# Performance work log

Measured on AMD Instinct MI355X. Metric: run time of the kernel, lower is better.

## Reference

```python
import jax, jax.numpy as jnp
import numpy as np
import math

BS, S, D = 2, 2048, 2048
DOWN, UP, H, RD = 512, 1024, 16, 32
HD = D // H            # 128, used only in softmax scale
VD = UP // H           # 64 per-head value dim
CD = UP // H           # 64 per-head content q/k dim
SCALE = math.sqrt(HD) + math.sqrt(RD)


def _rope(x, head_dim):
    # x: [bs, heads, seq, head_dim]; standard rotate-half RoPE
    seq = x.shape[2]
    inv_freq = 1.0 / (10000.0 ** (jnp.arange(0, head_dim, 2, dtype=jnp.float32) / head_dim))
    freqs = jnp.arange(seq, dtype=jnp.float32)[:, None] * inv_freq[None, :]  # [S, hd/2]
    emb = jnp.concatenate([freqs, freqs], axis=-1)                            # [S, hd]
    cos = jnp.cos(emb)[None, None]
    sin = jnp.sin(emb)[None, None]
    x1, x2 = x[..., : head_dim // 2], x[..., head_dim // 2 :]
    rot = jnp.concatenate([-x2, x1], axis=-1)
    return x * cos + rot * sin


def setup_inputs() -> dict:
    key = jax.random.key(0)
    ks = jax.random.split(key, 10)
    sd = 0.02
    inp = {
        'h': jax.random.normal(ks[0], (BS, S, D), jnp.float32),
        'mask': jnp.tril(jnp.ones((1, 1, S, S), jnp.int32)),
        'Wdkv': jax.random.normal(ks[1], (DOWN, D), jnp.float32) * sd,
        'bdkv': jnp.zeros((DOWN,), jnp.float32),
        'Wuk': jax.random.normal(ks[2], (UP, DOWN), jnp.float32) * sd,
        'buk': jnp.zeros((UP,), jnp.float32),
        'Wuv': jax.random.normal(ks[3], (UP, DOWN), jnp.float32) * sd,
        'buv': jnp.zeros((UP,), jnp.float32),
        'Wdq': jax.random.normal(ks[4], (DOWN, D), jnp.float32) * sd,
        'bdq': jnp.zeros((DOWN,), jnp.float32),
        'Wuq': jax.random.normal(ks[5], (UP, DOWN), jnp.float32) * sd,
        'buq': jnp.zeros((UP,), jnp.float32),
        'Wqr': jax.random.normal(ks[6], (RD * H, DOWN), jnp.float32) * sd,
        'bqr': jnp.zeros((RD * H,), jnp.float32),
        'Wkr': jax.random.normal(ks[7], (RD, D), jnp.float32) * sd,
        'bkr': jnp.zeros((RD,), jnp.float32),
        'Wfc': jax.random.normal(ks[8], (D, H * VD), jnp.float32) * sd,
        'bfc': jnp.zeros((D,), jnp.float32),
    }
    return inp


def reference(h, mask, Wdkv, bdkv, Wuk, buk, Wuv, buv, Wdq, bdq, Wuq, buq,
              Wqr, bqr, Wkr, bkr, Wfc, bfc):
    bs, seq, _ = h.shape
    # low-rank KV path
    c_kv = h @ Wdkv.T + bdkv                                   # [bs,S,DOWN]
    k_c = (c_kv @ Wuk.T + buk).reshape(bs, seq, H, CD).transpose(0, 2, 1, 3)
    v_c = (c_kv @ Wuv.T + buv).reshape(bs, seq, H, VD).transpose(0, 2, 1, 3)
    # low-rank Q path
    c_q = h @ Wdq.T + bdq                                      # [bs,S,DOWN]
    q_c = (c_q @ Wuq.T + buq).reshape(bs, seq, H, CD).transpose(0, 2, 1, 3)
    # decoupled RoPE paths
    q_r = _rope((c_q @ Wqr.T + bqr).reshape(bs, seq, H, RD).transpose(0, 2, 1, 3), RD)
    k_r = _rope((h @ Wkr.T + bkr).reshape(bs, seq, 1, RD).transpose(0, 2, 1, 3), RD)
    k_r = jnp.broadcast_to(k_r, (bs, H, seq, RD))              # shared RoPE key across heads
    q = jnp.concatenate([q_c, q_r], axis=-1)                   # [bs,H,S,CD+RD]
    k = jnp.concatenate([k_c, k_r], axis=-1)
    scores = jnp.einsum('bhqd,bhkd->bhqk', q, k)
    # NB: original applies mask BEFORE dividing by scale
    scores = jnp.where(mask == 0, -1e9, scores)
    probs = jax.nn.softmax(scores / SCALE, axis=-1)
    out = jnp.einsum('bhqk,bhkd->bhqd', probs, v_c)            # [bs,H,S,VD]
    out = out.transpose(0, 2, 1, 3).reshape(bs, seq, H * VD)
    return out @ Wfc.T + bfc
```

## Files before the change

### kernel.cpp

```cpp
#include <hip/hip_runtime.h>
#include <hip/hip_bf16.h>
#include <math.h>

typedef unsigned short u16;
typedef __attribute__((ext_vector_type(8))) short bf16x8;
typedef __attribute__((ext_vector_type(4))) float f32x4;
typedef __attribute__((ext_vector_type(16))) float f32x16;

namespace {

constexpr int BS = 2;
constexpr int S = 2048;
constexpr int D = 2048;
constexpr int DOWN = 512;
constexpr int UP = 1024;
constexpr int H = 16;
constexpr int RD = 32;
constexpr int VD = 64;
constexpr int QKD = 96;
constexpr int M = BS * S;
constexpr int N1 = 1152;
constexpr int N2 = 2048;
constexpr int N3 = 1536;

__device__ __forceinline__ float b2f(u16 u) {
  unsigned int x = ((unsigned int)u) << 16;
  return __uint_as_float(x);
}
__device__ __forceinline__ u16 f2b(float f) {
  unsigned int u = __float_as_uint(f);
  u += 0x7fff + ((u >> 16) & 1);
  return (u16)(u >> 16);
}
__device__ __forceinline__ void store_out(float* p, float v) { *p = v; }
__device__ __forceinline__ void store_out(u16* p, float v) { *p = f2b(v); }

__device__ __forceinline__ void async16(const u16* g, u16* lds) {
  __builtin_amdgcn_global_load_lds(
      (const __attribute__((address_space(1))) unsigned int*)g,
      (__attribute__((address_space(3))) unsigned int*)lds, 16, 0, 0);
}

__device__ __forceinline__ float exp2_fast(float x) {
#if __has_builtin(__builtin_amdgcn_exp2f)
  return __builtin_amdgcn_exp2f(x);
#else
  float r;
  asm("v_exp_f32 %0, %1" : "=v"(r) : "v"(x));
  return r;
#endif
}

__device__ __forceinline__ unsigned pkbf(float a, float b) {
  union { __hip_bfloat162 h; unsigned u; } c;
  c.h = __float22bfloat162_rn(make_float2(a, b));
  return c.u;
}
__device__ __forceinline__ void plswap(unsigned& a, unsigned& b) {
  asm("v_permlane32_swap_b32 %0, %1" : "+v"(a), "+v"(b));
}

__device__ __forceinline__ f32x4 mfma32(bf16x8 a, bf16x8 b, f32x4 c) {
  return __builtin_amdgcn_mfma_f32_16x16x32_bf16(a, b, c, 0, 0, 0);
}
__device__ __forceinline__ f32x16 mfma3216(bf16x8 a, bf16x8 b, f32x16 c) {
  return __builtin_amdgcn_mfma_f32_32x32x16_bf16(a, b, c, 0, 0, 0);
}

__global__ __launch_bounds__(256) void prep_kernel(
    const float* __restrict__ h, const float* __restrict__ Wdkv,
    const float* __restrict__ Wdq, const float* __restrict__ Wkr,
    const float* __restrict__ Wuk, const float* __restrict__ Wuv,
    const float* __restrict__ Wuq, const float* __restrict__ Wqr,
    const float* __restrict__ Wfc, const float* __restrict__ bdkv,
    const float* __restrict__ bdq, const float* __restrict__ bkr,
    const float* __restrict__ buk, const float* __restrict__ buv,
    const float* __restrict__ buq, const float* __restrict__ bqr,
    u16* __restrict__ hb, u16* __restrict__ Wcat1, u16* __restrict__ Wcat2,
    u16* __restrict__ Wcat3, u16* __restrict__ Wfcb,
    float* __restrict__ bcat1, float* __restrict__ bcat2,
    float* __restrict__ bcat3, float* __restrict__ ct, float* __restrict__ st) {
  const long i = (long)blockIdx.x * 256 + threadIdx.x;
  if (i >= 3630240) return;
  if (i < 3620864) {
    const float* src; u16* dst; long off;
    if      (i < 2097152) { src = h;    dst = hb;              off = i; }
    else if (i < 2359296) { src = Wdkv; dst = Wcat1;           off = i - 2097152; }
    else if (i < 2621440) { src = Wdq;  dst = Wcat1 + 1048576; off = i - 2359296; }
    else if (i < 2637824) { src = Wkr;  dst = Wcat1 + 2097152; off = i - 2621440; }
    else if (i < 2768896) { src = Wuk;  dst = Wcat2;           off = i - 2637824; }
    else if (i < 2899968) { src = Wuv;  dst = Wcat2 + 524288;  off = i - 2768896; }
    else if (i < 3031040) { src = Wuq;  dst = Wcat3;           off = i - 2899968; }
    else if (i < 3096576) { src = Wqr;  dst = Wcat3 + 524288;  off = i - 3031040; }
    else                  { src = Wfc;  dst = Wfcb;            off = i - 3096576; }
    float4 v = ((const float4*)src)[off];
    ushort4 o;
    o.x = f2b(v.x); o.y = f2b(v.y); o.z = f2b(v.z); o.w = f2b(v.w);
    ((ushort4*)dst)[off] = o;
  } else if (i < 3622048) {
    long j0 = (i - 3620864) * 4;
#pragma unroll
    for (int e = 0; e < 4; ++e) {
      long j = j0 + e;
      if (j < N1) {
        float v = 0.f;
        if (j < 512) v = bdkv[j];
        else if (j < 1024) v = bdq[j - 512];
        else if (j < 1056) v = bkr[j - 1024];
        bcat1[j] = v;
      } else if (j < N1 + N2) {
        long jj = j - N1;
        bcat2[jj] = (jj < 1024) ? buk[jj] : buv[jj - 1024];
      } else {
        long jj = j - N1 - N2;
        bcat3[jj] = (jj < 1024) ? buq[jj] : bqr[jj - 1024];
      }
    }
  } else {
    long k0 = (i - 3622048) * 4;
#pragma unroll
    for (int e = 0; e < 4; ++e) {
      long k = k0 + e;
      int s = (int)(k >> 4), r = (int)(k & 15);
      float f = powf(10000.f, -(float)r / 16.f);
      float th = (float)s * f;
      ct[k] = cosf(th);
      st[k] = sinf(th);
    }
  }
}

template <int BN, typename OutT>
__device__ __forceinline__ void gemm_body(
    const u16* __restrict__ A, int lda, const u16* __restrict__ W, int ldw,
    const float* __restrict__ bias, OutT* __restrict__ C, int ldc, int K,
    int m0, int n0) {
  constexpr int NFR = BN / 32;
  __shared__ u16 As[128 * 32];
  __shared__ u16 Bs[BN * 32];
  const int t = threadIdx.x;
  const int lane = t & 63, wave = t >> 6;
  const int wm = (wave >> 1) * 64, wn = (wave & 1) * (BN / 2);
  const int lrow = lane & 15, lk = (lane >> 4) * 8;
  const int srow = lane >> 2, scol = (lane & 3) * 8;
  f32x4 acc[4][NFR] = {};
  for (int k0 = 0; k0 < K; k0 += 32) {
    __syncthreads();
    {
      int r = wave * 32 + srow;
      async16(A + (size_t)(m0 + r) * lda + k0 + scol, As + (wave * 32) * 32);
      async16(A + (size_t)(m0 + r + 16) * lda + k0 + scol,
              As + (wave * 32 + 16) * 32);
    }
    if (BN == 128) {
      int r = wave * 32 + srow;
      async16(W + (size_t)(n0 + r) * ldw + k0 + scol, Bs + (wave * 32) * 32);
      async16(W + (size_t)(n0 + r + 16) * ldw + k0 + scol,
              Bs + (wave * 32 + 16) * 32);
    } else {
      int r = wave * 16 + srow;
      async16(W + (size_t)(n0 + r) * ldw + k0 + scol, Bs + (wave * 16) * 32);
    }
    __syncthreads();
    bf16x8 af[4], bfr[NFR];
#pragma unroll
    for (int i = 0; i < 4; ++i)
      af[i] = *(const bf16x8*)(As + (wm + i * 16 + lrow) * 32 + lk);
#pragma unroll
    for (int i = 0; i < NFR; ++i)
      bfr[i] = *(const bf16x8*)(Bs + (wn + i * 16 + lrow) * 32 + lk);
#pragma unroll
    for (int mi = 0; mi < 4; ++mi)
#pragma unroll
      for (int ni = 0; ni < NFR; ++ni)
        acc[mi][ni] = mfma32(af[mi], bfr[ni], acc[mi][ni]);
  }
#pragma unroll
  for (int mi = 0; mi < 4; ++mi)
#pragma unroll
    for (int ni = 0; ni < NFR; ++ni)
#pragma unroll
      for (int r = 0; r < 4; ++r) {
        int m = m0 + wm + mi * 16 + (lane >> 4) * 4 + r;
        int n = n0 + wn + ni * 16 + lrow;
        store_out(C + (size_t)m * ldc + n, acc[mi][ni][r] + bias[n]);
      }
}

template <int BN, typename OutT>
__global__ __launch_bounds__(256) void gemm_bt_mfma(
    const u16* __restrict__ A, int lda, const u16* __restrict__ W, int ldw,
    const float* __restrict__ bias, OutT* __restrict__ C, int ldc, int K) {
  gemm_body<BN, OutT>(A, lda, W, ldw, bias, C, ldc, K,
                      blockIdx.x * 128, blockIdx.y * BN);
}

__global__ __launch_bounds__(256) void gemm_up_fused(
    const u16* __restrict__ C1v, const u16* __restrict__ Wcat2,
    const u16* __restrict__ Wcat3, const float* __restrict__ bcat2,
    const float* __restrict__ bcat3, u16* __restrict__ C2,
    u16* __restrict__ C3) {
  const int by = blockIdx.y;
  const u16* A;
  const u16* W;
  const float* bias;
  u16* C;
  int ldc, n0;
  if (by < 16) {
    A = C1v; W = Wcat2; bias = bcat2; C = C2; ldc = N2; n0 = by * 128;
  } else {
    A = C1v + DOWN; W = Wcat3; bias = bcat3; C = C3; ldc = N3;
    n0 = (by - 16) * 128;
  }
  gemm_body<128, u16>(A, N1, W, DOWN, bias, C, ldc, DOWN,
                      blockIdx.x * 128, n0);
}

__global__ __launch_bounds__(256) void transpose_kernel(
    const u16* __restrict__ in, int ld_in, u16* __restrict__ outT, int ld_out) {
  __shared__ u16 tile[64][72];
  const int m0 = blockIdx.x * 64, n0 = blockIdx.y * 64;
  const int r = threadIdx.x >> 2, c0 = (threadIdx.x & 3) * 16;
  *(bf16x8*)(&tile[r][c0]) =
      *(const bf16x8*)(in + (size_t)(m0 + r) * ld_in + n0 + c0);
  *(bf16x8*)(&tile[r][c0 + 8]) =
      *(const bf16x8*)(in + (size_t)(m0 + r) * ld_in + n0 + c0 + 8);
  __syncthreads();
  bf16x8 o0, o1;
#pragma unroll
  for (int j = 0; j < 8; ++j) {
    o0[j] = (short)tile[c0 + j][r];
    o1[j] = (short)tile[c0 + 8 + j][r];
  }
  *(bf16x8*)(outT + (size_t)(n0 + r) * ld_out + m0 + c0) = o0;
  *(bf16x8*)(outT + (size_t)(n0 + r) * ld_out + m0 + c0 + 8) = o1;
}

__global__ __launch_bounds__(192) void pack_q_kernel(
    const u16* __restrict__ qc, const u16* __restrict__ qr,
    const float* __restrict__ ct, const float* __restrict__ st,
    u16* __restrict__ Qp) {
  const int t = threadIdx.x;
  const int sub = (t >= 96) ? 1 : 0;
  const int d = t - sub * 96;
  const int s = blockIdx.x * 2 + sub, h = blockIdx.y, b = blockIdx.z;
  const float sc = 1.44269504088896f / (sqrtf(128.f) + sqrtf(32.f));
  float val;
  if (d < 64) {
    val = b2f(qc[(size_t)(b * S + s) * N3 + h * VD + d]);
  } else {
    int r = d - 64;
    const u16* qrow = qr + (size_t)(b * S + s) * N3 + h * RD;
    float x = b2f(qrow[r]), xp = b2f(qrow[r ^ 16]);
    float c = ct[s * 16 + (r & 15)], sn = st[s * 16 + (r & 15)];
    val = (r < 16) ? (x * c - xp * sn) : (x * c + xp * sn);
  }
  Qp[((size_t)(b * H + h) * S + s) * QKD + d] = f2b(val * sc);
}

__global__ __launch_bounds__(192) void pack_k_kernel(
    const u16* __restrict__ kc,
    const u16* __restrict__ kr,
    const float* __restrict__ ct, const float* __restrict__ st,
    u16* __restrict__ Kp) {
  const int t = threadIdx.x;
  const int sub = (t >= 96) ? 1 : 0;
  const int d = t - sub * 96;
  const int s = blockIdx.x * 2 + sub, h = blockIdx.y, b = blockIdx.z;
  float val;
  if (d < 64) {
    val = b2f(kc[(size_t)(b * S + s) * N2 + h * VD + d]);
  } else {
    int r = d - 64;
    const u16* krow = kr + (size_t)(b * S + s) * N1;
    float x = b2f(krow[r]), xp = b2f(krow[r ^ 16]);
    float c = ct[s * 16 + (r & 15)], sn = st[s * 16 + (r & 15)];
    val = (r < 16) ? (x * c - xp * sn) : (x * c + xp * sn);
  }
  Kp[((size_t)(b * H + h) * S + s) * QKD + d] = f2b(val);
}

__global__ __launch_bounds__(256, 4) void attn_mfma(
    const u16* __restrict__ Qp, const u16* __restrict__ Kp,
    const u16* __restrict__ Vt, u16* __restrict__ attnb) {
  const int t = threadIdx.x, wave = t >> 6, lane = t & 63;
  const int l31 = lane & 31, hw = lane >> 5;
  const int bh = blockIdx.x & 31;
  const int b = bh >> 4, h = bh & 15;
  const int tile = 63 - (blockIdx.x >> 5);
  const int q0w = tile * 32;
  const size_t hbo = (size_t)bh * S;

  __shared__ float red[3][64][33];

  bf16x8 qf[6];
  {
    const u16* qrow = Qp + (hbo + q0w + l31) * QKD + hw * 8;
#pragma unroll
    for (int c = 0; c < 6; ++c) qf[c] = *(const bf16x8*)(qrow + c * 16);
  }
  f32x16 O0 = {0,0,0,0,0,0,0,0,0,0,0,0,0,0,0,0};
  f32x16 O1 = {0,0,0,0,0,0,0,0,0,0,0,0,0,0,0,0};
  float lsum = 0.f;
  const int q_abs = q0w + l31;
  const u16* vb0 = Vt + ((size_t)(h * VD + l31)) * M + (size_t)b * S + 8 * hw;

  bf16x8 kf[6];
  {
    const u16* kb = Kp + (hbo + wave * 32 + l31) * QKD + hw * 8;
#pragma unroll
    for (int c = 0; c < 6; ++c) kf[c] = *(const bf16x8*)(kb + c * 16);
  }

  for (int m = wave; m <= tile; m += 4) {
    const int k0 = m * 32;
    f32x16 s = {0,0,0,0,0,0,0,0,0,0,0,0,0,0,0,0};
#pragma unroll
    for (int c = 0; c < 6; ++c) s = mfma3216(kf[c], qf[c], s);
    if (m + 4 <= tile) {
      const u16* kb = Kp + (hbo + (size_t)(m + 4) * 32 + l31) * QKD + hw * 8;
#pragma unroll
      for (int c = 0; c < 6; ++c) kf[c] = *(const bf16x8*)(kb + c * 16);
    }
    bf16x8 vf00 = *(const bf16x8*)(vb0 + k0);
    bf16x8 vf01 = *(const bf16x8*)(vb0 + k0 + 16);
    bf16x8 vf10 = *(const bf16x8*)(vb0 + (size_t)32 * M + k0);
    bf16x8 vf11 = *(const bf16x8*)(vb0 + (size_t)32 * M + k0 + 16);
    if (m == tile) {
#pragma unroll
      for (int r = 0; r < 16; ++r) {
        int key_abs = k0 + (r & 3) + 8 * (r >> 2) + 4 * hw;
        float v = exp2_fast(s[r]);
        s[r] = (key_abs <= q_abs) ? v : 0.f;
      }
    } else {
#pragma unroll
      for (int r = 0; r < 16; ++r) s[r] = exp2_fast(s[r]);
    }
#pragma unroll
    for (int r = 0; r < 16; ++r) lsum += s[r];
    unsigned w0 = pkbf(s[0], s[1]),   w1 = pkbf(s[2], s[3]);
    unsigned w2 = pkbf(s[4], s[5]),   w3 = pkbf(s[6], s[7]);
    unsigned w4 = pkbf(s[8], s[9]),   w5 = pkbf(s[10], s[11]);
    unsigned w6 = pkbf(s[12], s[13]), w7 = pkbf(s[14], s[15]);
    plswap(w0, w2); plswap(w1, w3); plswap(w4, w6); plswap(w5, w7);
    union { unsigned u[4]; bf16x8 v; } ua, ub;
    ua.u[0] = w0; ua.u[1] = w1; ua.u[2] = w2; ua.u[3] = w3;
    ub.u[0] = w4; ub.u[1] = w5; ub.u[2] = w6; ub.u[3] = w7;
    O0 = mfma3216(ua.v, vf00, O0);
    O0 = mfma3216(ub.v, vf01, O0);
    O1 = mfma3216(ua.v, vf10, O1);
    O1 = mfma3216(ub.v, vf11, O1);
  }

  if (wave > 0) {
#pragma unroll
    for (int r = 0; r < 16; ++r) {
      red[wave - 1][lane][r] = O0[r];
      red[wave - 1][lane][16 + r] = O1[r];
    }
    red[wave - 1][lane][32] = lsum;
  }
  __syncthreads();
  if (wave == 0) {
#pragma unroll
    for (int w = 0; w < 3; ++w) {
#pragma unroll
      for (int r = 0; r < 16; ++r) {
        O0[r] += red[w][lane][r];
        O1[r] += red[w][lane][16 + r];
      }
      lsum += red[w][lane][32];
    }
    float tot = lsum + __shfl_xor(lsum, 32);
    u16* ob = attnb + (size_t)b * S * UP + h * VD;
#pragma unroll
    for (int r = 0; r < 16; ++r) {
      int rowq = (r & 3) + 8 * (r >> 2) + 4 * hw;
      float linv = 1.f / __shfl(tot, rowq);
      size_t rowoff = (size_t)(q0w + rowq) * UP;
      ob[rowoff + l31] = f2b(O0[r] * linv);
      ob[rowoff + 32 + l31] = f2b(O1[r] * linv);
    }
  }
}

}

extern "C" void kernel_launch(void* const* d_in, const int* in_sizes, int n_in,
                              void* d_out, int out_size, void* d_ws, size_t ws_size,
                              hipStream_t stream) {
  const float* h    = (const float*)d_in[0];
  const float* Wdkv = (const float*)d_in[2];
  const float* bdkv = (const float*)d_in[3];
  const float* Wuk  = (const float*)d_in[4];
  const float* buk  = (const float*)d_in[5];
  const float* Wuv  = (const float*)d_in[6];
  const float* buv  = (const float*)d_in[7];
  const float* Wdq  = (const float*)d_in[8];
  const float* bdq  = (const float*)d_in[9];
  const float* Wuq  = (const float*)d_in[10];
  const float* buq  = (const float*)d_in[11];
  const float* Wqr  = (const float*)d_in[12];
  const float* bqr  = (const float*)d_in[13];
  const float* Wkr  = (const float*)d_in[14];
  const float* bkr  = (const float*)d_in[15];
  const float* Wfc  = (const float*)d_in[16];
  const float* bfc  = (const float*)d_in[17];
  float* out = (float*)d_out;

  u16* p = (u16*)d_ws;
  u16* hb    = p; p += (size_t)M * D;
  u16* Wcat1 = p; p += (size_t)N1 * D;
  u16* Wcat2 = p; p += (size_t)N2 * DOWN;
  u16* Wcat3 = p; p += (size_t)N3 * DOWN;
  u16* Wfcb  = p; p += (size_t)D * UP;
  u16* C1    = p; p += (size_t)M * N1;
  u16* C2    = p; p += (size_t)M * N2;
  u16* C3    = p; p += (size_t)M * N3;
  u16* Qp    = p; p += 6291456;
  u16* Kp    = p; p += 6291456;
  u16* Vt    = p; p += (size_t)UP * M;
  float* bcat1 = (float*)p; p += 2 * N1;
  float* bcat2 = (float*)p; p += 2 * N2;
  float* bcat3 = (float*)p; p += 2 * N3;
  float* ct = (float*)p; p += 2 * S * 16;
  float* st = (float*)p; p += 2 * S * 16;
  u16* attnb = C1;

  prep_kernel<<<dim3(14181), 256, 0, stream>>>(
      h, Wdkv, Wdq, Wkr, Wuk, Wuv, Wuq, Wqr, Wfc,
      bdkv, bdq, bkr, buk, buv, buq, bqr,
      hb, Wcat1, Wcat2, Wcat3, Wfcb, bcat1, bcat2, bcat3, ct, st);

  gemm_bt_mfma<64, u16><<<dim3(M / 128, N1 / 64), 256, 0, stream>>>(
      hb, D, Wcat1, D, bcat1, C1, N1, D);
  gemm_up_fused<<<dim3(M / 128, 28), 256, 0, stream>>>(
      C1, Wcat2, Wcat3, bcat2, bcat3, C2, C3);

  pack_q_kernel<<<dim3(S / 2, H, BS), 192, 0, stream>>>(
      C3, C3 + UP, ct, st, Qp);
  pack_k_kernel<<<dim3(S / 2, H, BS), 192, 0, stream>>>(
      C2, C1 + 2 * DOWN, ct, st, Kp);
  transpose_kernel<<<dim3(M / 64, UP / 64), 256, 0, stream>>>(
      C2 + UP, N2, Vt, M);

  attn_mfma<<<dim3(2048), 256, 0, stream>>>(Qp, Kp, Vt, attnb);

  gemm_bt_mfma<64, float><<<dim3(M / 128, D / 64), 256, 0, stream>>>(
      attnb, UP, Wfcb, UP, bfc, out, D, UP);
}
```

Baseline: 346.8 us.

## Block V transpose per key tile and split QK MFMA accumulator chains

The transposed V layout changes to a per-(batch,head) blocked format where each 32-key tile's 64x32 slab is contiguous, so attention V loads come from one contiguous 4KB block instead of rows strided by M. In the attention loop, V loads are issued before the QK MFMAs to hide latency. The six dependent QK MFMAs are split into two independent accumulators that are summed before exp, and the PV MFMAs are interleaved. Launch bounds drop occupancy from 4 to 3 waves per SIMD to give the extra accumulator registers room, at the cost of some latency hiding.

New measurement: 318.3 us. -8.2%, faster.

```diff
diff --git a/kernel.cpp b/kernel.cpp
--- a/kernel.cpp
+++ b/kernel.cpp
@@ -216,15 +216,16 @@
                       blockIdx.x * 128, n0);
 }
 
-__global__ __launch_bounds__(256) void transpose_kernel(
-    const u16* __restrict__ in, int ld_in, u16* __restrict__ outT, int ld_out) {
+__global__ __launch_bounds__(256) void transpose_v_kernel(
+    const u16* __restrict__ in, int ld_in, u16* __restrict__ VtB) {
   __shared__ u16 tile[64][72];
-  const int m0 = blockIdx.x * 64, n0 = blockIdx.y * 64;
+  const int m0 = blockIdx.x * 64;
+  const int h = blockIdx.y;
   const int r = threadIdx.x >> 2, c0 = (threadIdx.x & 3) * 16;
   *(bf16x8*)(&tile[r][c0]) =
-      *(const bf16x8*)(in + (size_t)(m0 + r) * ld_in + n0 + c0);
+      *(const bf16x8*)(in + (size_t)(m0 + r) * ld_in + h * VD + c0);
   *(bf16x8*)(&tile[r][c0 + 8]) =
-      *(const bf16x8*)(in + (size_t)(m0 + r) * ld_in + n0 + c0 + 8);
+      *(const bf16x8*)(in + (size_t)(m0 + r) * ld_in + h * VD + c0 + 8);
   __syncthreads();
   bf16x8 o0, o1;
 #pragma unroll
@@ -232,8 +233,11 @@
     o0[j] = (short)tile[c0 + j][r];
     o1[j] = (short)tile[c0 + 8 + j][r];
   }
-  *(bf16x8*)(outT + (size_t)(n0 + r) * ld_out + m0 + c0) = o0;
-  *(bf16x8*)(outT + (size_t)(n0 + r) * ld_out + m0 + c0 + 8) = o1;
+  const int b = m0 / S, sb = m0 % S;
+  size_t dst = ((size_t)(b * H + h) * 64 + ((sb + c0) >> 5)) * 2048 +
+               (size_t)r * 32 + ((sb + c0) & 31);
+  *(bf16x8*)(VtB + dst) = o0;
+  *(bf16x8*)(VtB + dst + 8) = o1;
 }
 
 __global__ __launch_bounds__(192) void pack_q_kernel(
@@ -280,7 +284,7 @@
   Kp[((size_t)(b * H + h) * S + s) * QKD + d] = f2b(val);
 }
 
-__global__ __launch_bounds__(256, 4) void attn_mfma(
+__global__ __launch_bounds__(256, 3) void attn_mfma(
     const u16* __restrict__ Qp, const u16* __restrict__ Kp,
     const u16* __restrict__ Vt, u16* __restrict__ attnb) {
   const int t = threadIdx.x, wave = t >> 6, lane = t & 63;
@@ -303,7 +307,7 @@
   f32x16 O1 = {0,0,0,0,0,0,0,0,0,0,0,0,0,0,0,0};
   float lsum = 0.f;
   const int q_abs = q0w + l31;
-  const u16* vb0 = Vt + ((size_t)(h * VD + l31)) * M + (size_t)b * S + 8 * hw;
+  const u16* vbase = Vt + (size_t)bh * 64 * 2048 + l31 * 32 + 8 * hw;
 
   bf16x8 kf[6];
   {
@@ -314,42 +318,54 @@
 
   for (int m = wave; m <= tile; m += 4) {
     const int k0 = m * 32;
-    f32x16 s = {0,0,0,0,0,0,0,0,0,0,0,0,0,0,0,0};
-#pragma unroll
-    for (int c = 0; c < 6; ++c) s = mfma3216(kf[c], qf[c], s);
+    const u16* vb = vbase + (size_t)m * 2048;
+    bf16x8 vf00 = *(const bf16x8*)(vb);
+    bf16x8 vf01 = *(const bf16x8*)(vb + 16);
+    bf16x8 vf10 = *(const bf16x8*)(vb + 1024);
+    bf16x8 vf11 = *(const bf16x8*)(vb + 1024 + 16);
+    f32x16 sa = {0,0,0,0,0,0,0,0,0,0,0,0,0,0,0,0};
+    f32x16 sb = {0,0,0,0,0,0,0,0,0,0,0,0,0,0,0,0};
+    sa = mfma3216(kf[0], qf[0], sa);
+    sb = mfma3216(kf[1], qf[1], sb);
+    sa = mfma3216(kf[2], qf[2], sa);
+    sb = mfma3216(kf[3], qf[3], sb);
+    sa = mfma3216(kf[4], qf[4], sa);
+    sb = mfma3216(kf[5], qf[5], sb);
     if (m + 4 <= tile) {
       const u16* kb = Kp + (hbo + (size_t)(m + 4) * 32 + l31) * QKD + hw * 8;
 #pragma unroll
       for (int c = 0; c < 6; ++c) kf[c] = *(const bf16x8*)(kb + c * 16);
     }
-    bf16x8 vf00 = *(const bf16x8*)(vb0 + k0);
-    bf16x8 vf01 = *(const bf16x8*)(vb0 + k0 + 16);
-    bf16x8 vf10 = *(const bf16x8*)(vb0 + (size_t)32 * M + k0);
-    bf16x8 vf11 = *(const bf16x8*)(vb0 + (size_t)32 * M + k0 + 16);
+    float e[16];
     if (m == tile) {
 #pragma unroll
       for (int r = 0; r < 16; ++r) {
         int key_abs = k0 + (r & 3) + 8 * (r >> 2) + 4 * hw;
-        float v = exp2_fast(s[r]);
-        s[r] = (key_abs <= q_abs) ? v : 0.f;
+        float v = exp2_fast(sa[r] + sb[r]);
+        e[r] = (key_abs <= q_abs) ? v : 0.f;
       }
     } else {
 #pragma unroll
-      for (int r = 0; r < 16; ++r) s[r] = exp2_fast(s[r]);
-    }
-#pragma unroll
-    for (int r = 0; r < 16; ++r) lsum += s[r];
-    unsigned w0 = pkbf(s[0], s[1]),   w1 = pkbf(s[2], s[3]);
-    unsigned w2 = pkbf(s[4], s[5]),   w3 = pkbf(s[6], s[7]);
-    unsigned w4 = pkbf(s[8], s[9]),   w5 = pkbf(s[10], s[11]);
-    unsigned w6 = pkbf(s[12], s[13]), w7 = pkbf(s[14], s[15]);
+      for (int r = 0; r < 16; ++r) e[r] = exp2_fast(sa[r] + sb[r]);
+    }
+    {
+      float p0 = (e[0] + e[1]) + (e[2] + e[3]);
+      float p1 = (e[4] + e[5]) + (e[6] + e[7]);
+      float p2 = (e[8] + e[9]) + (e[10] + e[11]);
+      float p3 = (e[12] + e[13]) + (e[14] + e[15]);
+      lsum += (p0 + p1) + (p2 + p3);
+    }
+    unsigned w0 = pkbf(e[0], e[1]),   w1 = pkbf(e[2], e[3]);
+    unsigned w2 = pkbf(e[4], e[5]),   w3 = pkbf(e[6], e[7]);
+    unsigned w4 = pkbf(e[8], e[9]),   w5 = pkbf(e[10], e[11]);
+    unsigned w6 = pkbf(e[12], e[13]), w7 = pkbf(e[14], e[15]);
     plswap(w0, w2); plswap(w1, w3); plswap(w4, w6); plswap(w5, w7);
     union { unsigned u[4]; bf16x8 v; } ua, ub;
     ua.u[0] = w0; ua.u[1] = w1; ua.u[2] = w2; ua.u[3] = w3;
     ub.u[0] = w4; ub.u[1] = w5; ub.u[2] = w6; ub.u[3] = w7;
     O0 = mfma3216(ua.v, vf00, O0);
+    O1 = mfma3216(ua.v, vf10, O1);
     O0 = mfma3216(ub.v, vf01, O0);
-    O1 = mfma3216(ua.v, vf10, O1);
     O1 = mfma3216(ub.v, vf11, O1);
   }
 
@@ -442,8 +458,8 @@
       C3, C3 + UP, ct, st, Qp);
   pack_k_kernel<<<dim3(S / 2, H, BS), 192, 0, stream>>>(
       C2, C1 + 2 * DOWN, ct, st, Kp);
-  transpose_kernel<<<dim3(M / 64, UP / 64), 256, 0, stream>>>(
-      C2 + UP, N2, Vt, M);
+  transpose_v_kernel<<<dim3(M / 64, UP / 64), 256, 0, stream>>>(
+      C2 + UP, N2, Vt);
 
   attn_mfma<<<dim3(2048), 256, 0, stream>>>(Qp, Kp, Vt, attnb);
 
```
